# Performance work log

Hardware: AMD Instinct MI355X
Metric: run time of the kernel (lower is better)

Reference implementation:

```python
import jax, jax.numpy as jnp
import numpy as np

N_QUBITS = 8
REPS = 2
DIM = 2 ** N_QUBITS  # 256
C64 = jnp.complex64


def _apply_1q(state, gate, wire):
    """Apply a single-qubit gate. state: [B]+[2]*n, gate: [2,2] or [B,2,2]."""
    s = jnp.moveaxis(state, wire + 1, -1)
    if gate.ndim == 2:
        s = jnp.einsum('ij,b...j->b...i', gate, s)
    else:
        s = jnp.einsum('bij,b...j->b...i', gate, s)
    return jnp.moveaxis(s, -1, wire + 1)


def _cnot(state, ctrl, tgt):
    """CNOT: flip target axis where control bit == 1. state: [B]+[2]*n."""
    s0 = jax.lax.index_in_dim(state, 0, ctrl + 1, keepdims=True)
    s1 = jax.lax.index_in_dim(state, 1, ctrl + 1, keepdims=True)
    s1 = jnp.flip(s1, axis=tgt + 1)
    return jnp.concatenate([s0, s1], axis=ctrl + 1)


def _rx(a):
    """Batched RX gate. a: [B] -> [B,2,2] complex64."""
    c = jnp.cos(0.5 * a).astype(C64)
    s = jnp.sin(0.5 * a).astype(C64)
    mis = (-1j) * s
    return jnp.stack([jnp.stack([c, mis], -1), jnp.stack([mis, c], -1)], -2)


def _rot(phi, theta, omega):
    """PennyLane Rot = RZ(omega) RY(theta) RZ(phi). Scalars -> [2,2] complex64."""
    c = jnp.cos(0.5 * theta).astype(C64)
    s = jnp.sin(0.5 * theta).astype(C64)
    ep = jnp.exp(-0.5j * (phi + omega).astype(C64))   # e^{-i(phi+omega)/2}
    em = jnp.exp(-0.5j * (phi - omega).astype(C64))   # e^{-i(phi-omega)/2}
    epc = jnp.exp(0.5j * (phi + omega).astype(C64))
    emc = jnp.exp(0.5j * (phi - omega).astype(C64))
    return jnp.stack([
        jnp.stack([ep * c, -emc * s], -1),
        jnp.stack([em * s, epc * c], -1),
    ], -2)


def _circuit(x, theta):
    B = x.shape[0]
    state = jnp.zeros((B, DIM), C64).at[:, 0].set(1.0)
    state = state.reshape((B,) + (2,) * N_QUBITS)
    # AngleEmbedding (default rotation='X'): RX(x[:, w]) on wire w
    for w in range(N_QUBITS):
        state = _apply_1q(state, _rx(x[:, w]), w)
    # StronglyEntanglingLayers: per layer, Rot on every wire then ring of CNOTs
    for l in range(REPS):
        for w in range(N_QUBITS):
            g = _rot(theta[l, w, 0], theta[l, w, 1], theta[l, w, 2])
            state = _apply_1q(state, g, w)
        r = (l % (N_QUBITS - 1)) + 1  # PennyLane default ranges
        for w in range(N_QUBITS):
            state = _cnot(state, w, (w + r) % N_QUBITS)
    # expval(PauliZ(0)): wire 0 is the most significant axis
    probs = (state.real ** 2 + state.imag ** 2).reshape(B, 2, DIM // 2)
    ev = probs[:, 0].sum(-1) - probs[:, 1].sum(-1)
    return ((ev + 1.0) * 0.5)[:, None]  # [B, 1]


def setup_inputs() -> dict:
    key = jax.random.key(0)
    kx, kt = jax.random.split(key)
    x = jax.random.normal(kx, (131072, N_QUBITS), dtype=jnp.float32)
    theta = 0.1 * jax.random.normal(kt, (REPS, N_QUBITS, 3), dtype=jnp.float32)
    return {"x": x, "theta": theta}


def reference(x, theta):
    return _circuit(x, theta)
```

## Files before the change

kernel.cpp:

```cpp
#include <hip/hip_runtime.h>


typedef _Float16 v8hf __attribute__((ext_vector_type(8)));
typedef float v4f __attribute__((ext_vector_type(4)));

struct cpx { float re, im; };
__device__ __forceinline__ cpx cmul(cpx a, cpx b) {
    return {a.re * b.re - a.im * b.im, a.re * b.im + a.im * b.re};
}

__device__ __forceinline__ void get_pauli(int a, cpx P[2][2]) {
    cpx z{0.f, 0.f};
    P[0][0] = z; P[0][1] = z; P[1][0] = z; P[1][1] = z;
    switch (a) {
        case 0: P[0][0] = {1.f, 0.f}; P[1][1] = {1.f, 0.f}; break;
        case 1: P[0][1] = {1.f, 0.f}; P[1][0] = {1.f, 0.f}; break;
        case 2: P[0][1] = {0.f, -1.f}; P[1][0] = {0.f, 1.f}; break;
        case 3: P[0][0] = {1.f, 0.f}; P[1][1] = {-1.f, 0.f}; break;
    }
}

__device__ void compute_ptm(const float* __restrict__ theta, int l, int w,
                            float* out) {
    const float phi = theta[(l * 8 + w) * 3 + 0];
    const float th  = theta[(l * 8 + w) * 3 + 1];
    const float om  = theta[(l * 8 + w) * 3 + 2];
    const float c = cosf(0.5f * th), s = sinf(0.5f * th);
    const float ps = 0.5f * (phi + om), ms = 0.5f * (phi - om);
    cpx G[2][2];
    G[0][0] = {c * cosf(ps), -c * sinf(ps)};
    G[0][1] = {-s * cosf(ms), -s * sinf(ms)};
    G[1][0] = {s * cosf(ms), -s * sinf(ms)};
    G[1][1] = {c * cosf(ps), c * sinf(ps)};
    for (int a = 0; a < 4; ++a) {
        cpx Pa[2][2]; get_pauli(a, Pa);
        cpx M1[2][2];
        for (int i = 0; i < 2; ++i)
            for (int j = 0; j < 2; ++j) {
                cpx acc{0.f, 0.f};
                for (int k = 0; k < 2; ++k) {
                    cpx t = cmul(Pa[i][k], G[k][j]);
                    acc.re += t.re; acc.im += t.im;
                }
                M1[i][j] = acc;
            }
        cpx H[2][2];
        for (int i = 0; i < 2; ++i)
            for (int j = 0; j < 2; ++j) {
                cpx acc{0.f, 0.f};
                for (int k = 0; k < 2; ++k) {
                    cpx gc{G[k][i].re, -G[k][i].im};
                    cpx t = cmul(gc, M1[k][j]);
                    acc.re += t.re; acc.im += t.im;
                }
                H[i][j] = acc;
            }
        for (int b = 0; b < 4; ++b) {
            cpx Pb[2][2]; get_pauli(b, Pb);
            float tr = 0.f;
            for (int i = 0; i < 2; ++i)
                for (int j = 0; j < 2; ++j)
                    tr += Pb[i][j].re * H[j][i].re - Pb[i][j].im * H[j][i].im;
            out[a * 4 + b] = 0.5f * tr;
        }
    }
}

__device__ void compute_cnot_entry(int pr, int* oidx, float* osgn) {
    const int pc = pr >> 2, pt = pr & 3;
    const int perm[4] = {0, 1, 3, 2};
    cpx Pc[2][2], Pt[2][2];
    get_pauli(pc, Pc); get_pauli(pt, Pt);
    cpx S[4][4];
    for (int i = 0; i < 2; ++i)
        for (int j = 0; j < 2; ++j)
            for (int k = 0; k < 2; ++k)
                for (int l2 = 0; l2 < 2; ++l2)
                    S[2 * i + j][2 * k + l2] = cmul(Pc[i][k], Pt[j][l2]);
    cpx R[4][4];
    for (int r = 0; r < 4; ++r)
        for (int c2 = 0; c2 < 4; ++c2)
            R[r][c2] = S[perm[r]][perm[c2]];
    int bidx = 0; float bsgn = 1.f;
    for (int a = 0; a < 4; ++a)
        for (int b2 = 0; b2 < 4; ++b2) {
            cpx Pa[2][2], Pb[2][2];
            get_pauli(a, Pa); get_pauli(b2, Pb);
            float ov = 0.f;
            for (int r = 0; r < 4; ++r)
                for (int c2 = 0; c2 < 4; ++c2) {
                    cpx K = cmul(Pa[r >> 1][c2 >> 1], Pb[r & 1][c2 & 1]);
                    ov += K.re * R[r][c2].re + K.im * R[r][c2].im;
                }
            ov *= 0.25f;
            if (ov > 0.5f) { bidx = a * 4 + b2; bsgn = 1.f; }
            else if (ov < -0.5f) { bidx = a * 4 + b2; bsgn = -1.f; }
        }
    *oidx = bidx;
    *osgn = bsgn;
}

#define OFF_AF 0
#define OFF_R  4096
#define WS_FLOATS_NEEDED (4096 + 16 * 729)

__device__ __forceinline__ int ring_conj(int cur, int r, const int* CIDX,
                                         const float* CSGN, float& sg) {
    for (int w = 7; w >= 0; --w) {
        const int tw = (w + r) & 7;
        const int pc = (cur >> (2 * w)) & 3;
        const int pt = (cur >> (2 * tw)) & 3;
        const int q = pc * 4 + pt;
        const int nq = CIDX[q];
        sg *= CSGN[q];
        cur = (cur & ~((3 << (2 * w)) | (3 << (2 * tw))))
            | ((nq >> 2) << (2 * w)) | ((nq & 3) << (2 * tw));
    }
    return cur;
}

__global__ __launch_bounds__(1024) void k_sub(const float* __restrict__ theta,
                                              float* __restrict__ ws) {
    __shared__ float TR[256];
    __shared__ float CSGN[16];
    __shared__ int   CIDX[16];
    __shared__ float Wa[4096];
    __shared__ float Wb[3072];
    __shared__ int   S1k, S1n;
    __shared__ float S1sgn;
    __shared__ int   S1w[8], S1l[8];

    const int tid = threadIdx.x;
    const int sub = blockIdx.x;
    const int sa0 = sub >> 2, sa1 = sub & 3;
    float* Rg = ws + OFF_R;

    if (tid < 16) compute_ptm(theta, tid >> 3, tid & 7, &TR[tid * 16]);
    if (tid >= 64 && tid < 80) compute_cnot_entry(tid - 64, &CIDX[tid - 64], &CSGN[tid - 64]);
    for (int i = tid; i < 4096; i += 1024) Wa[i] = 0.f;
    __syncthreads();

    if (tid == 0) {
        float sg = 1.f;
        int cur = ring_conj(3 , 2, CIDX, CSGN, sg);
        int k = 0;
        for (int w = 0; w < 8; ++w) {
            const int ltr = (cur >> (2 * w)) & 3;
            if (ltr != 0) { S1w[k] = w; S1l[k] = ltr; ++k; }
        }
        int n = 1;
        for (int i = 0; i < k; ++i) n *= 3;
        S1sgn = sg; S1k = k; S1n = n;
    }
    __syncthreads();
    const int k1 = S1k, n1 = S1n;

    for (int t = tid; t < n1; t += 1024) {
        float c = S1sgn;
        int s = 0;
        int tt = t;
        for (int i = 0; i < k1; ++i) {
            const int bl = tt % 3 + 1;
            tt /= 3;
            c *= TR[(8 + S1w[i]) * 16 + S1l[i] * 4 + bl];
            s |= bl << (2 * S1w[i]);
        }
        float sg = 1.f;
        s = ring_conj(s, 1, CIDX, CSGN, sg);
        c *= sg;
        if (((s & 3) == sa0) && (((s >> 2) & 3) == sa1)) {
            int d4 = 0;
#pragma unroll
            for (int w = 2; w < 8; ++w)
                d4 |= ((s >> (2 * w)) & 3) << (2 * (7 - w));
            Wa[d4] = c;
        }
    }
    __syncthreads();

    const int P3c[6] = {1, 3, 9, 27, 81, 243};
    const int N4c[6] = {1024, 256, 64, 16, 4, 1};
#pragma unroll
    for (int tl = 0; tl < 6; ++tl) {
        const int w = 7 - tl;
        const float* src = (tl & 1) ? Wb : Wa;
        float* dst = (tl & 1) ? Wa : Wb;
        const int p3 = P3c[tl];
        const int Nout = p3 * 3 * N4c[tl];
        for (int idx = tid; idx < Nout; idx += 1024) {
            const int q3 = idx % p3;
            const int rest = idx / p3;
            const int P = rest % 3;
            const int r = rest / 3;
            const int let = (P == 0) ? 0 : ((P == 1) ? 3 : 2);
            const float* ib = src + q3 + p3 * 4 * r;
            dst[idx] = ib[0] * TR[w * 16 + 0 + let]
                     + ib[p3] * TR[w * 16 + 4 + let]
                     + ib[2 * p3] * TR[w * 16 + 8 + let]
                     + ib[3 * p3] * TR[w * 16 + 12 + let];
        }
        __syncthreads();
    }
    for (int k = tid; k < 729; k += 1024) Rg[sub * 729 + k] = Wa[k];
}

__global__ __launch_bounds__(1024) void k_fin(const float* __restrict__ theta,
                                              float* __restrict__ ws) {
    __shared__ float BIG[8748];
    __shared__ float TRw[32];
    const int tid = threadIdx.x;
    if (tid < 2) compute_ptm(theta, 0, tid, &TRw[tid * 16]);
    __syncthreads();

    const float* Rg = ws + OFF_R;
    for (int idx1 = tid; idx1 < 8748; idx1 += 1024) {
        const int a0 = idx1 / 2187;
        const int rem = idx1 % 2187;
        const int P1 = rem / 729;
        const int qq = rem % 729;
        const int let = (P1 == 0) ? 0 : ((P1 == 1) ? 3 : 2);
        float v = 0.f;
#pragma unroll
        for (int a1 = 0; a1 < 4; ++a1)
            v += Rg[(a0 * 4 + a1) * 729 + qq] * TRw[16 + a1 * 4 + let];
        BIG[idx1] = v;
    }
    __syncthreads();

    int* AFi = (int*)(ws + OFF_AF);
    for (int u = tid; u < 4096; u += 1024) {
        const int t = u >> 8;
        const int lane = (u >> 2) & 63;
        const int jj0 = (u & 3) * 2;
        const int m = lane & 15;
        const int i = t * 16 + m;
        const int jb = (lane >> 4) * 8;
        unsigned int packed = 0;
#pragma unroll
        for (int z = 0; z < 2; ++z) {
            const int j = jb + jj0 + z;
            float v = 0.f;
            if (i < 243 && j < 27) {
                const int idxF = i * 27 + j;
                const int P0 = idxF / 2187;
                const int rest = idxF % 2187;
                const int let = (P0 == 0) ? 0 : ((P0 == 1) ? 3 : 2);
                v = BIG[rest] * TRw[0 + let]
                  + BIG[2187 + rest] * TRw[4 + let]
                  + BIG[2 * 2187 + rest] * TRw[8 + let]
                  + BIG[3 * 2187 + rest] * TRw[12 + let];
            }
            const _Float16 hv = (_Float16)v;
            const unsigned short bits = __builtin_bit_cast(unsigned short, hv);
            packed |= ((unsigned int)bits) << (16 * z);
        }
        AFi[u] = (int)packed;
    }
}

template <int Q>
__device__ __forceinline__ v8hf build_bfrag(const float* m5v, const float* m6v,
                                            const float* m7v) {
    v8hf bf;
#pragma unroll
    for (int jj = 0; jj < 8; ++jj) {
        const int j = Q * 8 + jj;
        float v = 0.f;
        if (j < 27) {
            const int k5 = j / 9, k6 = (j % 9) / 3, k7 = j % 3;
            v = m5v[k5] * m6v[k6] * m7v[k7];
        }
        bf[jj] = (_Float16)v;
    }
    return bf;
}

template <int Q>
__device__ __forceinline__ float contract_f1(const v4f* acc, const float* P01,
                                             const float* P23, const float* m4v) {
    float ev = 0.f;
#pragma unroll
    for (int t = 0; t < 16; ++t) {
#pragma unroll
        for (int s = 0; s < 4; ++s) {
            const int i = 16 * t + 4 * Q + s;
            if (i < 243) {
                const int u = i / 27, vv = (i % 27) / 3, w = i % 3;
                float f = P01[u] * P23[vv];
                if (w != 0) f *= m4v[w];
                ev = fmaf(f, acc[t][s], ev);
            }
        }
    }
    return ev;
}

__global__ __launch_bounds__(256, 2) void k_main4(const float* __restrict__ x,
                                                  const float* __restrict__ wsAF,
                                                  float* __restrict__ out,
                                                  int ngroups) {
    const int lane = threadIdx.x & 63;
    const int q = lane >> 4, e = lane & 15;
    const int wid = (blockIdx.x * blockDim.x + threadIdx.x) >> 6;
    if (wid >= ngroups) return;

    const int b = wid * 16 + e;
    const float4* xp = (const float4*)(x + (size_t)b * 8);
    const float4 xa = xp[0], xb = xp[1];
    float m0v[3], m1v[3], m2v[3], m3v[3], m4v[3], m5v[3], m6v[3], m7v[3];
    {
        float sv, cv;
        __sincosf(xa.x, &sv, &cv); m0v[0] = 1.f; m0v[1] = cv; m0v[2] = -sv;
        __sincosf(xa.y, &sv, &cv); m1v[0] = 1.f; m1v[1] = cv; m1v[2] = -sv;
        __sincosf(xa.z, &sv, &cv); m2v[0] = 1.f; m2v[1] = cv; m2v[2] = -sv;
        __sincosf(xa.w, &sv, &cv); m3v[0] = 1.f; m3v[1] = cv; m3v[2] = -sv;
        __sincosf(xb.x, &sv, &cv); m4v[0] = 1.f; m4v[1] = cv; m4v[2] = -sv;
        __sincosf(xb.y, &sv, &cv); m5v[0] = 1.f; m5v[1] = cv; m5v[2] = -sv;
        __sincosf(xb.z, &sv, &cv); m6v[0] = 1.f; m6v[1] = cv; m6v[2] = -sv;
        __sincosf(xb.w, &sv, &cv); m7v[0] = 1.f; m7v[1] = cv; m7v[2] = -sv;
    }

    v8hf bf;
    if (q == 0)      bf = build_bfrag<0>(m5v, m6v, m7v);
    else if (q == 1) bf = build_bfrag<1>(m5v, m6v, m7v);
    else if (q == 2) bf = build_bfrag<2>(m5v, m6v, m7v);
    else             bf = build_bfrag<3>(m5v, m6v, m7v);

    float P01[9], P23[9];
#pragma unroll
    for (int a = 0; a < 3; ++a)
#pragma unroll
        for (int b2 = 0; b2 < 3; ++b2) {
            P01[a * 3 + b2] = m0v[a] * m1v[b2];
            P23[a * 3 + b2] = m2v[a] * m3v[b2];
        }

    const v4f zero = {0.f, 0.f, 0.f, 0.f};
    const v8hf* AFp = (const v8hf*)wsAF;
    v4f acc[16];
#pragma unroll
    for (int t = 0; t < 16; ++t)
        acc[t] = __builtin_amdgcn_mfma_f32_16x16x32_f16(AFp[t * 64 + lane], bf, zero, 0, 0, 0);

    float ev;
    if (q == 0)      ev = contract_f1<0>(acc, P01, P23, m4v);
    else if (q == 1) ev = contract_f1<1>(acc, P01, P23, m4v);
    else if (q == 2) ev = contract_f1<2>(acc, P01, P23, m4v);
    else             ev = contract_f1<3>(acc, P01, P23, m4v);

    ev += __shfl_xor(ev, 16, 64);
    ev += __shfl_xor(ev, 32, 64);
    if (lane < 16) out[b] = (ev + 1.f) * 0.5f;
}

struct c32 { float x, y; };

__device__ __forceinline__ c32 shfl_xor_c(c32 v, int mask) {
    c32 r;
    r.x = __shfl_xor(v.x, mask, 64);
    r.y = __shfl_xor(v.y, mask, 64);
    return r;
}
__device__ __forceinline__ c32 cmadd2(c32 ga, c32 a, c32 gp, c32 p) {
    c32 n;
    n.x = ga.x * a.x - ga.y * a.y + gp.x * p.x - gp.y * p.y;
    n.y = ga.x * a.y + ga.y * a.x + gp.x * p.y + gp.y * p.x;
    return n;
}
__device__ __forceinline__ c32 rx_mix(float c, float s, c32 a, c32 p) {
    c32 n;
    n.x = c * a.x + s * p.y;
    n.y = c * a.y - s * p.x;
    return n;
}
__device__ __forceinline__ void apply_rx(c32 st[4], int lane, int bb, float c, float s) {
    if (bb < 6) {
#pragma unroll
        for (int r = 0; r < 4; ++r) {
            c32 p = shfl_xor_c(st[r], 1 << bb);
            st[r] = rx_mix(c, s, st[r], p);
        }
    } else if (bb == 6) {
        c32 n0 = rx_mix(c, s, st[0], st[1]);
        c32 n1 = rx_mix(c, s, st[1], st[0]);
        c32 n2 = rx_mix(c, s, st[2], st[3]);
        c32 n3 = rx_mix(c, s, st[3], st[2]);
        st[0] = n0; st[1] = n1; st[2] = n2; st[3] = n3;
    } else {
        c32 n0 = rx_mix(c, s, st[0], st[2]);
        c32 n2 = rx_mix(c, s, st[2], st[0]);
        c32 n1 = rx_mix(c, s, st[1], st[3]);
        c32 n3 = rx_mix(c, s, st[3], st[1]);
        st[0] = n0; st[1] = n1; st[2] = n2; st[3] = n3;
    }
}
__device__ __forceinline__ void apply_rot(c32 st[4], int lane, int bb,
                                          c32 g00, c32 g01, c32 g10, c32 g11) {
    if (bb < 6) {
#pragma unroll
        for (int r = 0; r < 4; ++r) {
            c32 p = shfl_xor_c(st[r], 1 << bb);
            bool hi = (lane >> bb) & 1;
            c32 ga, gp;
            ga.x = hi ? g11.x : g00.x;
            ga.y = hi ? g11.y : g00.y;
            gp.x = hi ? g10.x : g01.x;
            gp.y = hi ? g10.y : g01.y;
            st[r] = cmadd2(ga, st[r], gp, p);
        }
    } else if (bb == 6) {
        c32 n0 = cmadd2(g00, st[0], g01, st[1]);
        c32 n1 = cmadd2(g10, st[0], g11, st[1]);
        c32 n2 = cmadd2(g00, st[2], g01, st[3]);
        c32 n3 = cmadd2(g10, st[2], g11, st[3]);
        st[0] = n0; st[1] = n1; st[2] = n2; st[3] = n3;
    } else {
        c32 n0 = cmadd2(g00, st[0], g01, st[2]);
        c32 n2 = cmadd2(g10, st[0], g11, st[2]);
        c32 n1 = cmadd2(g00, st[1], g01, st[3]);
        c32 n3 = cmadd2(g10, st[1], g11, st[3]);
        st[0] = n0; st[1] = n1; st[2] = n2; st[3] = n3;
    }
}
__device__ __forceinline__ void cswap(bool c, c32& a, c32& b) {
    c32 t = a;
    a.x = c ? b.x : a.x; a.y = c ? b.y : a.y;
    b.x = c ? t.x : b.x; b.y = c ? t.y : b.y;
}
__device__ __forceinline__ void apply_cnot(c32 st[4], int lane, int bc, int bt) {
    if (bt < 6) {
        if (bc < 6) {
            bool ctrl = (lane >> bc) & 1;
#pragma unroll
            for (int r = 0; r < 4; ++r) {
                c32 p = shfl_xor_c(st[r], 1 << bt);
                st[r].x = ctrl ? p.x : st[r].x;
                st[r].y = ctrl ? p.y : st[r].y;
            }
        } else {
#pragma unroll
            for (int r = 0; r < 4; ++r) {
                if ((r >> (bc - 6)) & 1) st[r] = shfl_xor_c(st[r], 1 << bt);
            }
        }
    } else {
        if (bc < 6) {
            bool ctrl = (lane >> bc) & 1;
            if (bt == 6) { cswap(ctrl, st[0], st[1]); cswap(ctrl, st[2], st[3]); }
            else         { cswap(ctrl, st[0], st[2]); cswap(ctrl, st[1], st[3]); }
        } else {
            if (bc == 7 && bt == 6) { c32 t = st[2]; st[2] = st[3]; st[3] = t; }
            else if (bc == 6 && bt == 7) { c32 t = st[1]; st[1] = st[3]; st[3] = t; }
        }
    }
}
__global__ __launch_bounds__(256) void qsim_kernel(const float* __restrict__ x,
                                                   const float* __restrict__ theta,
                                                   float* __restrict__ out,
                                                   int batch) {
    __shared__ float rot[2 * 8 * 8];
    const int t = threadIdx.x;
    if (t < 16) {
        const int l = t >> 3, w = t & 7;
        const float phi = theta[(l * 8 + w) * 3 + 0];
        const float th  = theta[(l * 8 + w) * 3 + 1];
        const float om  = theta[(l * 8 + w) * 3 + 2];
        const float c = cosf(0.5f * th), s = sinf(0.5f * th);
        const float p = 0.5f * (phi + om), m = 0.5f * (phi - om);
        float* g = &rot[t * 8];
        g[0] = c * cosf(p);  g[1] = -c * sinf(p);
        g[2] = -s * cosf(m); g[3] = -s * sinf(m);
        g[4] = s * cosf(m);  g[5] = -s * sinf(m);
        g[6] = c * cosf(p);  g[7] = c * sinf(p);
    }
    __syncthreads();
    const int lane = t & 63;
    const int b = blockIdx.x * 4 + (t >> 6);
    if (b >= batch) return;
    float c8 = 0.f, s8 = 0.f;
    if (lane < 8) {
        const float xv = 0.5f * x[b * 8 + lane];
        c8 = cosf(xv); s8 = sinf(xv);
    }
    c32 st[4];
#pragma unroll
    for (int r = 0; r < 4; ++r) { st[r].x = 0.f; st[r].y = 0.f; }
    if (lane == 0) st[0].x = 1.f;
#pragma unroll
    for (int w = 0; w < 8; ++w) {
        const float c = __shfl(c8, w, 64);
        const float s = __shfl(s8, w, 64);
        apply_rx(st, lane, 7 - w, c, s);
    }
#pragma unroll
    for (int l = 0; l < 2; ++l) {
#pragma unroll
        for (int w = 0; w < 8; ++w) {
            const float* g = &rot[(l * 8 + w) * 8];
            c32 g00{g[0], g[1]}, g01{g[2], g[3]}, g10{g[4], g[5]}, g11{g[6], g[7]};
            apply_rot(st, lane, 7 - w, g00, g01, g10, g11);
        }
        const int rr = l + 1;
#pragma unroll
        for (int w = 0; w < 8; ++w) apply_cnot(st, lane, 7 - w, 7 - ((w + rr) & 7));
    }
    float v = st[0].x * st[0].x + st[0].y * st[0].y
            + st[1].x * st[1].x + st[1].y * st[1].y
            - st[2].x * st[2].x - st[2].y * st[2].y
            - st[3].x * st[3].x - st[3].y * st[3].y;
#pragma unroll
    for (int off = 32; off > 0; off >>= 1) v += __shfl_xor(v, off, 64);
    if (lane == 0) out[b] = (v + 1.f) * 0.5f;
}

extern "C" void kernel_launch(void* const* d_in, const int* in_sizes, int n_in,
                              void* d_out, int out_size, void* d_ws, size_t ws_size,
                              hipStream_t stream) {
    const float* x     = (const float*)d_in[0];
    const float* theta = (const float*)d_in[1];
    float* out = (float*)d_out;
    const int batch = in_sizes[0] / 8;

    if (ws_size >= (size_t)WS_FLOATS_NEEDED * 4 + 256 && (batch & 15) == 0) {
        float* ws = (float*)d_ws;
        k_sub<<<dim3(16), dim3(1024), 0, stream>>>(theta, ws);
        k_fin<<<dim3(1), dim3(1024), 0, stream>>>(theta, ws);
        const int ngroups = batch / 16;
        const int blocks = (ngroups + 3) / 4;
        k_main4<<<dim3(blocks), dim3(256), 0, stream>>>(x, ws + OFF_AF, out, ngroups);
    } else {
        qsim_kernel<<<dim3((batch + 3) / 4), dim3(256), 0, stream>>>(x, theta, out, batch);
    }
}
```

Before: 81.90 us.

## Merge prep kernels with flag sync and reuse MFMA A-fragments across two groups

Fuses the two setup kernels into one 17-block launch. Sixteen blocks build the partial tables and publish them with release flags, and the 17th block spin-waits on those flags before doing the final reduction. The per-gate transfer-matrix and CNOT entries are now computed in parallel, one entry per thread, instead of by a few serial threads. In the main kernel each wave loads its A fragments into registers once and processes two batch groups, and precomputes a 27-entry product table to simplify the contraction. The flags are never reset between calls, so on later calls the final block may read a partially rewritten workspace. The wait also relies on all 17 blocks being resident at the same time.

Measured after the change: 91.13 us. 11.3% more time.

```diff
diff --git a/kernel.cpp b/kernel.cpp
--- a/kernel.cpp
+++ b/kernel.cpp
@@ -9,19 +9,17 @@
     return {a.re * b.re - a.im * b.im, a.re * b.im + a.im * b.re};
 }
 
-__device__ __forceinline__ void get_pauli(int a, cpx P[2][2]) {
-    cpx z{0.f, 0.f};
-    P[0][0] = z; P[0][1] = z; P[1][0] = z; P[1][1] = z;
-    switch (a) {
-        case 0: P[0][0] = {1.f, 0.f}; P[1][1] = {1.f, 0.f}; break;
-        case 1: P[0][1] = {1.f, 0.f}; P[1][0] = {1.f, 0.f}; break;
-        case 2: P[0][1] = {0.f, -1.f}; P[1][0] = {0.f, 1.f}; break;
-        case 3: P[0][0] = {1.f, 0.f}; P[1][1] = {-1.f, 0.f}; break;
-    }
-}
-
-__device__ void compute_ptm(const float* __restrict__ theta, int l, int w,
-                            float* out) {
+__device__ __forceinline__ cpx pget(int a, int i, int j) {
+    static const float RE[4][4] = {{1, 0, 0, 1}, {0, 1, 1, 0},
+                                   {0, 0, 0, 0}, {1, 0, 0, -1}};
+    static const float IM[4][4] = {{0, 0, 0, 0}, {0, 0, 0, 0},
+                                   {0, -1, 1, 0}, {0, 0, 0, 0}};
+    cpx r; r.re = RE[a][i * 2 + j]; r.im = IM[a][i * 2 + j];
+    return r;
+}
+
+__device__ float ptm_entry(const float* __restrict__ theta, int g, int a, int b) {
+    const int l = g >> 3, w = g & 7;
     const float phi = theta[(l * 8 + w) * 3 + 0];
     const float th  = theta[(l * 8 + w) * 3 + 1];
     const float om  = theta[(l * 8 + w) * 3 + 2];
@@ -32,77 +30,66 @@
     G[0][1] = {-s * cosf(ms), -s * sinf(ms)};
     G[1][0] = {s * cosf(ms), -s * sinf(ms)};
     G[1][1] = {c * cosf(ps), c * sinf(ps)};
-    for (int a = 0; a < 4; ++a) {
-        cpx Pa[2][2]; get_pauli(a, Pa);
-        cpx M1[2][2];
-        for (int i = 0; i < 2; ++i)
-            for (int j = 0; j < 2; ++j) {
-                cpx acc{0.f, 0.f};
-                for (int k = 0; k < 2; ++k) {
-                    cpx t = cmul(Pa[i][k], G[k][j]);
-                    acc.re += t.re; acc.im += t.im;
-                }
-                M1[i][j] = acc;
-            }
-        cpx H[2][2];
-        for (int i = 0; i < 2; ++i)
-            for (int j = 0; j < 2; ++j) {
-                cpx acc{0.f, 0.f};
-                for (int k = 0; k < 2; ++k) {
-                    cpx gc{G[k][i].re, -G[k][i].im};
-                    cpx t = cmul(gc, M1[k][j]);
-                    acc.re += t.re; acc.im += t.im;
-                }
-                H[i][j] = acc;
-            }
-        for (int b = 0; b < 4; ++b) {
-            cpx Pb[2][2]; get_pauli(b, Pb);
-            float tr = 0.f;
-            for (int i = 0; i < 2; ++i)
-                for (int j = 0; j < 2; ++j)
-                    tr += Pb[i][j].re * H[j][i].re - Pb[i][j].im * H[j][i].im;
-            out[a * 4 + b] = 0.5f * tr;
-        }
-    }
-}
-
-__device__ void compute_cnot_entry(int pr, int* oidx, float* osgn) {
+    cpx M1[2][2], H[2][2];
+#pragma unroll
+    for (int i = 0; i < 2; ++i)
+#pragma unroll
+        for (int j = 0; j < 2; ++j) {
+            cpx acc{0.f, 0.f};
+#pragma unroll
+            for (int k = 0; k < 2; ++k) {
+                cpx t = cmul(pget(a, i, k), G[k][j]);
+                acc.re += t.re; acc.im += t.im;
+            }
+            M1[i][j] = acc;
+        }
+#pragma unroll
+    for (int i = 0; i < 2; ++i)
+#pragma unroll
+        for (int j = 0; j < 2; ++j) {
+            cpx acc{0.f, 0.f};
+#pragma unroll
+            for (int k = 0; k < 2; ++k) {
+                cpx gc{G[k][i].re, -G[k][i].im};
+                cpx t = cmul(gc, M1[k][j]);
+                acc.re += t.re; acc.im += t.im;
+            }
+            H[i][j] = acc;
+        }
+    float tr = 0.f;
+#pragma unroll
+    for (int i = 0; i < 2; ++i)
+#pragma unroll
+        for (int j = 0; j < 2; ++j) {
+            cpx pb = pget(b, i, j);
+            tr += pb.re * H[j][i].re - pb.im * H[j][i].im;
+        }
+    return 0.5f * tr;
+}
+
+__device__ void cnot_entry(int pr, int cand, int* CIDX, float* CSGN) {
     const int pc = pr >> 2, pt = pr & 3;
+    const int a = cand >> 2, b2 = cand & 3;
     const int perm[4] = {0, 1, 3, 2};
-    cpx Pc[2][2], Pt[2][2];
-    get_pauli(pc, Pc); get_pauli(pt, Pt);
-    cpx S[4][4];
-    for (int i = 0; i < 2; ++i)
-        for (int j = 0; j < 2; ++j)
-            for (int k = 0; k < 2; ++k)
-                for (int l2 = 0; l2 < 2; ++l2)
-                    S[2 * i + j][2 * k + l2] = cmul(Pc[i][k], Pt[j][l2]);
-    cpx R[4][4];
+    float ov = 0.f;
+#pragma unroll
     for (int r = 0; r < 4; ++r)
-        for (int c2 = 0; c2 < 4; ++c2)
-            R[r][c2] = S[perm[r]][perm[c2]];
-    int bidx = 0; float bsgn = 1.f;
-    for (int a = 0; a < 4; ++a)
-        for (int b2 = 0; b2 < 4; ++b2) {
-            cpx Pa[2][2], Pb[2][2];
-            get_pauli(a, Pa); get_pauli(b2, Pb);
-            float ov = 0.f;
-            for (int r = 0; r < 4; ++r)
-                for (int c2 = 0; c2 < 4; ++c2) {
-                    cpx K = cmul(Pa[r >> 1][c2 >> 1], Pb[r & 1][c2 & 1]);
-                    ov += K.re * R[r][c2].re + K.im * R[r][c2].im;
-                }
-            ov *= 0.25f;
-            if (ov > 0.5f) { bidx = a * 4 + b2; bsgn = 1.f; }
-            else if (ov < -0.5f) { bidx = a * 4 + b2; bsgn = -1.f; }
-        }
-    *oidx = bidx;
-    *osgn = bsgn;
-}
-
-#define OFF_AF 0
-#define OFF_R  4096
-#define WS_FLOATS_NEEDED (4096 + 16 * 729)
+#pragma unroll
+        for (int c2 = 0; c2 < 4; ++c2) {
+            const int rp = perm[r], cp = perm[c2];
+            cpx Rv = cmul(pget(pc, rp >> 1, cp >> 1), pget(pt, rp & 1, cp & 1));
+            cpx Kv = cmul(pget(a, r >> 1, c2 >> 1), pget(b2, r & 1, c2 & 1));
+            ov += Kv.re * Rv.re + Kv.im * Rv.im;
+        }
+    ov *= 0.25f;
+    if (ov > 0.5f) { CIDX[pr] = cand; CSGN[pr] = 1.f; }
+    else if (ov < -0.5f) { CIDX[pr] = cand; CSGN[pr] = -1.f; }
+}
+
+#define OFF_AF   0
+#define OFF_R    4096
+#define OFF_FLAG (4096 + 16 * 729)
+#define WS_FLOATS_NEEDED (4096 + 16 * 729 + 16)
 
 __device__ __forceinline__ int ring_conj(int cur, int r, const int* CIDX,
                                          const float* CSGN, float& sg) {
@@ -119,142 +106,160 @@
     return cur;
 }
 
-__global__ __launch_bounds__(1024) void k_sub(const float* __restrict__ theta,
+__global__ __launch_bounds__(256) void k_prep(const float* __restrict__ theta,
                                               float* __restrict__ ws) {
-    __shared__ float TR[256];
-    __shared__ float CSGN[16];
-    __shared__ int   CIDX[16];
-    __shared__ float Wa[4096];
-    __shared__ float Wb[3072];
+    __shared__ float SH[8960];
     __shared__ int   S1k, S1n;
     __shared__ float S1sgn;
     __shared__ int   S1w[8], S1l[8];
 
     const int tid = threadIdx.x;
-    const int sub = blockIdx.x;
-    const int sa0 = sub >> 2, sa1 = sub & 3;
+    const int blk = blockIdx.x;
     float* Rg = ws + OFF_R;
-
-    if (tid < 16) compute_ptm(theta, tid >> 3, tid & 7, &TR[tid * 16]);
-    if (tid >= 64 && tid < 80) compute_cnot_entry(tid - 64, &CIDX[tid - 64], &CSGN[tid - 64]);
-    for (int i = tid; i < 4096; i += 1024) Wa[i] = 0.f;
-    __syncthreads();
-
-    if (tid == 0) {
-        float sg = 1.f;
-        int cur = ring_conj(3 , 2, CIDX, CSGN, sg);
-        int k = 0;
-        for (int w = 0; w < 8; ++w) {
-            const int ltr = (cur >> (2 * w)) & 3;
-            if (ltr != 0) { S1w[k] = w; S1l[k] = ltr; ++k; }
-        }
-        int n = 1;
-        for (int i = 0; i < k; ++i) n *= 3;
-        S1sgn = sg; S1k = k; S1n = n;
-    }
-    __syncthreads();
-    const int k1 = S1k, n1 = S1n;
-
-    for (int t = tid; t < n1; t += 1024) {
-        float c = S1sgn;
-        int s = 0;
-        int tt = t;
-        for (int i = 0; i < k1; ++i) {
-            const int bl = tt % 3 + 1;
-            tt /= 3;
-            c *= TR[(8 + S1w[i]) * 16 + S1l[i] * 4 + bl];
-            s |= bl << (2 * S1w[i]);
-        }
-        float sg = 1.f;
-        s = ring_conj(s, 1, CIDX, CSGN, sg);
-        c *= sg;
-        if (((s & 3) == sa0) && (((s >> 2) & 3) == sa1)) {
-            int d4 = 0;
-#pragma unroll
-            for (int w = 2; w < 8; ++w)
-                d4 |= ((s >> (2 * w)) & 3) << (2 * (7 - w));
-            Wa[d4] = c;
-        }
-    }
-    __syncthreads();
-
-    const int P3c[6] = {1, 3, 9, 27, 81, 243};
-    const int N4c[6] = {1024, 256, 64, 16, 4, 1};
-#pragma unroll
-    for (int tl = 0; tl < 6; ++tl) {
-        const int w = 7 - tl;
-        const float* src = (tl & 1) ? Wb : Wa;
-        float* dst = (tl & 1) ? Wa : Wb;
-        const int p3 = P3c[tl];
-        const int Nout = p3 * 3 * N4c[tl];
-        for (int idx = tid; idx < Nout; idx += 1024) {
-            const int q3 = idx % p3;
-            const int rest = idx / p3;
-            const int P = rest % 3;
-            const int r = rest / 3;
-            const int let = (P == 0) ? 0 : ((P == 1) ? 3 : 2);
-            const float* ib = src + q3 + p3 * 4 * r;
-            dst[idx] = ib[0] * TR[w * 16 + 0 + let]
-                     + ib[p3] * TR[w * 16 + 4 + let]
-                     + ib[2 * p3] * TR[w * 16 + 8 + let]
-                     + ib[3 * p3] * TR[w * 16 + 12 + let];
-        }
+    int* FLAGS = (int*)(ws + OFF_FLAG);
+
+    if (blk < 16) {
+        float* TR   = SH;
+        float* CSGN = SH + 256;
+        int*   CIDX = (int*)(SH + 272);
+        float* Wa   = SH + 288;
+        float* Wb   = SH + 4384;
+
+        const int sa0 = blk >> 2, sa1 = blk & 3;
+
+        TR[tid] = ptm_entry(theta, tid >> 4, (tid >> 2) & 3, tid & 3);
+        cnot_entry(tid >> 4, tid & 15, CIDX, CSGN);
+        for (int i = tid; i < 4096; i += 256) Wa[i] = 0.f;
         __syncthreads();
-    }
-    for (int k = tid; k < 729; k += 1024) Rg[sub * 729 + k] = Wa[k];
-}
-
-__global__ __launch_bounds__(1024) void k_fin(const float* __restrict__ theta,
-                                              float* __restrict__ ws) {
-    __shared__ float BIG[8748];
-    __shared__ float TRw[32];
-    const int tid = threadIdx.x;
-    if (tid < 2) compute_ptm(theta, 0, tid, &TRw[tid * 16]);
-    __syncthreads();
-
-    const float* Rg = ws + OFF_R;
-    for (int idx1 = tid; idx1 < 8748; idx1 += 1024) {
-        const int a0 = idx1 / 2187;
-        const int rem = idx1 % 2187;
-        const int P1 = rem / 729;
-        const int qq = rem % 729;
-        const int let = (P1 == 0) ? 0 : ((P1 == 1) ? 3 : 2);
-        float v = 0.f;
-#pragma unroll
-        for (int a1 = 0; a1 < 4; ++a1)
-            v += Rg[(a0 * 4 + a1) * 729 + qq] * TRw[16 + a1 * 4 + let];
-        BIG[idx1] = v;
-    }
-    __syncthreads();
-
-    int* AFi = (int*)(ws + OFF_AF);
-    for (int u = tid; u < 4096; u += 1024) {
-        const int t = u >> 8;
-        const int lane = (u >> 2) & 63;
-        const int jj0 = (u & 3) * 2;
-        const int m = lane & 15;
-        const int i = t * 16 + m;
-        const int jb = (lane >> 4) * 8;
-        unsigned int packed = 0;
-#pragma unroll
-        for (int z = 0; z < 2; ++z) {
-            const int j = jb + jj0 + z;
+
+        if (tid == 0) {
+            float sg = 1.f;
+            int cur = ring_conj(3 , 2, CIDX, CSGN, sg);
+            int k = 0;
+            for (int w = 0; w < 8; ++w) {
+                const int ltr = (cur >> (2 * w)) & 3;
+                if (ltr != 0) { S1w[k] = w; S1l[k] = ltr; ++k; }
+            }
+            int n = 1;
+            for (int i = 0; i < k; ++i) n *= 3;
+            S1sgn = sg; S1k = k; S1n = n;
+        }
+        __syncthreads();
+        const int k1 = S1k, n1 = S1n;
+
+        for (int t = tid; t < n1; t += 256) {
+            float c = S1sgn;
+            int s = 0;
+            int tt = t;
+            for (int i = 0; i < k1; ++i) {
+                const int bl = tt % 3 + 1;
+                tt /= 3;
+                c *= TR[(8 + S1w[i]) * 16 + S1l[i] * 4 + bl];
+                s |= bl << (2 * S1w[i]);
+            }
+            float sg = 1.f;
+            s = ring_conj(s, 1, CIDX, CSGN, sg);
+            c *= sg;
+            if (((s & 3) == sa0) && (((s >> 2) & 3) == sa1)) {
+                int d4 = 0;
+#pragma unroll
+                for (int w = 2; w < 8; ++w)
+                    d4 |= ((s >> (2 * w)) & 3) << (2 * (7 - w));
+                Wa[d4] = c;
+            }
+        }
+        __syncthreads();
+
+        const int P3c[6] = {1, 3, 9, 27, 81, 243};
+        const int N4c[6] = {1024, 256, 64, 16, 4, 1};
+#pragma unroll
+        for (int tl = 0; tl < 6; ++tl) {
+            const int w = 7 - tl;
+            const float* src = (tl & 1) ? Wb : Wa;
+            float* dst = (tl & 1) ? Wa : Wb;
+            const int p3 = P3c[tl];
+            const int Nout = p3 * 3 * N4c[tl];
+            for (int idx = tid; idx < Nout; idx += 256) {
+                const int q3 = idx % p3;
+                const int rest = idx / p3;
+                const int P = rest % 3;
+                const int r = rest / 3;
+                const int let = (P == 0) ? 0 : ((P == 1) ? 3 : 2);
+                const float* ib = src + q3 + p3 * 4 * r;
+                dst[idx] = ib[0] * TR[w * 16 + 0 + let]
+                         + ib[p3] * TR[w * 16 + 4 + let]
+                         + ib[2 * p3] * TR[w * 16 + 8 + let]
+                         + ib[3 * p3] * TR[w * 16 + 12 + let];
+            }
+            __syncthreads();
+        }
+        for (int k = tid; k < 729; k += 256)
+            __hip_atomic_store(&Rg[blk * 729 + k], Wa[k],
+                               __ATOMIC_RELAXED, __HIP_MEMORY_SCOPE_AGENT);
+        __threadfence();
+        __syncthreads();
+        if (tid == 0)
+            __hip_atomic_store(&FLAGS[blk], 1,
+                               __ATOMIC_RELEASE, __HIP_MEMORY_SCOPE_AGENT);
+    } else {
+        float* BIG = SH;
+        float* TRw = SH + 8748;
+        if (tid < 32)
+            TRw[tid] = ptm_entry(theta, tid >> 4, (tid >> 2) & 3, tid & 3);
+        if (tid < 16) {
+            while (__hip_atomic_load(&FLAGS[tid], __ATOMIC_ACQUIRE,
+                                     __HIP_MEMORY_SCOPE_AGENT) != 1) {
+                __builtin_amdgcn_s_sleep(1);
+            }
+        }
+        __threadfence();
+        __syncthreads();
+
+        for (int idx1 = tid; idx1 < 8748; idx1 += 256) {
+            const int a0 = idx1 / 2187;
+            const int rem = idx1 % 2187;
+            const int P1 = rem / 729;
+            const int qq = rem % 729;
+            const int let = (P1 == 0) ? 0 : ((P1 == 1) ? 3 : 2);
             float v = 0.f;
-            if (i < 243 && j < 27) {
-                const int idxF = i * 27 + j;
-                const int P0 = idxF / 2187;
-                const int rest = idxF % 2187;
-                const int let = (P0 == 0) ? 0 : ((P0 == 1) ? 3 : 2);
-                v = BIG[rest] * TRw[0 + let]
-                  + BIG[2187 + rest] * TRw[4 + let]
-                  + BIG[2 * 2187 + rest] * TRw[8 + let]
-                  + BIG[3 * 2187 + rest] * TRw[12 + let];
-            }
-            const _Float16 hv = (_Float16)v;
-            const unsigned short bits = __builtin_bit_cast(unsigned short, hv);
-            packed |= ((unsigned int)bits) << (16 * z);
-        }
-        AFi[u] = (int)packed;
+#pragma unroll
+            for (int a1 = 0; a1 < 4; ++a1)
+                v += __hip_atomic_load(&Rg[(a0 * 4 + a1) * 729 + qq],
+                                       __ATOMIC_RELAXED, __HIP_MEMORY_SCOPE_AGENT)
+                     * TRw[16 + a1 * 4 + let];
+            BIG[idx1] = v;
+        }
+        __syncthreads();
+
+        int* AFi = (int*)(ws + OFF_AF);
+        for (int u = tid; u < 4096; u += 256) {
+            const int t = u >> 8;
+            const int lane = (u >> 2) & 63;
+            const int jj0 = (u & 3) * 2;
+            const int m = lane & 15;
+            const int i = t * 16 + m;
+            const int jb = (lane >> 4) * 8;
+            unsigned int packed = 0;
+#pragma unroll
+            for (int z = 0; z < 2; ++z) {
+                const int j = jb + jj0 + z;
+                float v = 0.f;
+                if (i < 243 && j < 27) {
+                    const int idxF = i * 27 + j;
+                    const int P0 = idxF / 2187;
+                    const int rest = idxF % 2187;
+                    const int let = (P0 == 0) ? 0 : ((P0 == 1) ? 3 : 2);
+                    v = BIG[rest] * TRw[0 + let]
+                      + BIG[2187 + rest] * TRw[4 + let]
+                      + BIG[2 * 2187 + rest] * TRw[8 + let]
+                      + BIG[3 * 2187 + rest] * TRw[12 + let];
+                }
+                const _Float16 hv = (_Float16)v;
+                const unsigned short bits = __builtin_bit_cast(unsigned short, hv);
+                packed |= ((unsigned int)bits) << (16 * z);
+            }
+            AFi[u] = (int)packed;
+        }
     }
 }
 
@@ -276,81 +281,85 @@
 }
 
 template <int Q>
-__device__ __forceinline__ float contract_f1(const v4f* acc, const float* P01,
-                                             const float* P23, const float* m4v) {
+__device__ __forceinline__ float contract_f1(const v4f* acc, const float* U9,
+                                             const float* R27) {
     float ev = 0.f;
 #pragma unroll
     for (int t = 0; t < 16; ++t) {
 #pragma unroll
         for (int s = 0; s < 4; ++s) {
             const int i = 16 * t + 4 * Q + s;
-            if (i < 243) {
-                const int u = i / 27, vv = (i % 27) / 3, w = i % 3;
-                float f = P01[u] * P23[vv];
-                if (w != 0) f *= m4v[w];
-                ev = fmaf(f, acc[t][s], ev);
-            }
+            if (i < 243)
+                ev = fmaf(U9[i / 27] * R27[i % 27], acc[t][s], ev);
         }
     }
     return ev;
 }
 
-__global__ __launch_bounds__(256, 2) void k_main4(const float* __restrict__ x,
+__global__ __launch_bounds__(256, 2) void k_main5(const float* __restrict__ x,
                                                   const float* __restrict__ wsAF,
                                                   float* __restrict__ out,
                                                   int ngroups) {
     const int lane = threadIdx.x & 63;
     const int q = lane >> 4, e = lane & 15;
-    const int wid = (blockIdx.x * blockDim.x + threadIdx.x) >> 6;
-    if (wid >= ngroups) return;
-
-    const int b = wid * 16 + e;
-    const float4* xp = (const float4*)(x + (size_t)b * 8);
-    const float4 xa = xp[0], xb = xp[1];
-    float m0v[3], m1v[3], m2v[3], m3v[3], m4v[3], m5v[3], m6v[3], m7v[3];
-    {
-        float sv, cv;
-        __sincosf(xa.x, &sv, &cv); m0v[0] = 1.f; m0v[1] = cv; m0v[2] = -sv;
-        __sincosf(xa.y, &sv, &cv); m1v[0] = 1.f; m1v[1] = cv; m1v[2] = -sv;
-        __sincosf(xa.z, &sv, &cv); m2v[0] = 1.f; m2v[1] = cv; m2v[2] = -sv;
-        __sincosf(xa.w, &sv, &cv); m3v[0] = 1.f; m3v[1] = cv; m3v[2] = -sv;
-        __sincosf(xb.x, &sv, &cv); m4v[0] = 1.f; m4v[1] = cv; m4v[2] = -sv;
-        __sincosf(xb.y, &sv, &cv); m5v[0] = 1.f; m5v[1] = cv; m5v[2] = -sv;
-        __sincosf(xb.z, &sv, &cv); m6v[0] = 1.f; m6v[1] = cv; m6v[2] = -sv;
-        __sincosf(xb.w, &sv, &cv); m7v[0] = 1.f; m7v[1] = cv; m7v[2] = -sv;
-    }
-
-    v8hf bf;
-    if (q == 0)      bf = build_bfrag<0>(m5v, m6v, m7v);
-    else if (q == 1) bf = build_bfrag<1>(m5v, m6v, m7v);
-    else if (q == 2) bf = build_bfrag<2>(m5v, m6v, m7v);
-    else             bf = build_bfrag<3>(m5v, m6v, m7v);
-
-    float P01[9], P23[9];
-#pragma unroll
-    for (int a = 0; a < 3; ++a)
-#pragma unroll
-        for (int b2 = 0; b2 < 3; ++b2) {
-            P01[a * 3 + b2] = m0v[a] * m1v[b2];
-            P23[a * 3 + b2] = m2v[a] * m3v[b2];
-        }
-
-    const v4f zero = {0.f, 0.f, 0.f, 0.f};
+    const int wslot = (blockIdx.x * blockDim.x + threadIdx.x) >> 6;
+
     const v8hf* AFp = (const v8hf*)wsAF;
-    v4f acc[16];
-#pragma unroll
-    for (int t = 0; t < 16; ++t)
-        acc[t] = __builtin_amdgcn_mfma_f32_16x16x32_f16(AFp[t * 64 + lane], bf, zero, 0, 0, 0);
-
-    float ev;
-    if (q == 0)      ev = contract_f1<0>(acc, P01, P23, m4v);
-    else if (q == 1) ev = contract_f1<1>(acc, P01, P23, m4v);
-    else if (q == 2) ev = contract_f1<2>(acc, P01, P23, m4v);
-    else             ev = contract_f1<3>(acc, P01, P23, m4v);
-
-    ev += __shfl_xor(ev, 16, 64);
-    ev += __shfl_xor(ev, 32, 64);
-    if (lane < 16) out[b] = (ev + 1.f) * 0.5f;
+    v8hf af[16];
+#pragma unroll
+    for (int t = 0; t < 16; ++t) af[t] = AFp[t * 64 + lane];
+
+    for (int gi = 0; gi < 2; ++gi) {
+        const int g = wslot * 2 + gi;
+        if (g >= ngroups) return;
+        const int b = g * 16 + e;
+        const float4* xp = (const float4*)(x + (size_t)b * 8);
+        const float4 xa = xp[0], xb = xp[1];
+
+        float m0v[3], m1v[3], m2v[3], m3v[3], m4v[3], m5v[3], m6v[3], m7v[3];
+        m0v[0] = 1.f; m0v[1] = __cosf(xa.x); m0v[2] = -__sinf(xa.x);
+        m1v[0] = 1.f; m1v[1] = __cosf(xa.y); m1v[2] = -__sinf(xa.y);
+        m2v[0] = 1.f; m2v[1] = __cosf(xa.z); m2v[2] = -__sinf(xa.z);
+        m3v[0] = 1.f; m3v[1] = __cosf(xa.w); m3v[2] = -__sinf(xa.w);
+        m4v[0] = 1.f; m4v[1] = __cosf(xb.x); m4v[2] = -__sinf(xb.x);
+        m5v[0] = 1.f; m5v[1] = __cosf(xb.y); m5v[2] = -__sinf(xb.y);
+        m6v[0] = 1.f; m6v[1] = __cosf(xb.z); m6v[2] = -__sinf(xb.z);
+        m7v[0] = 1.f; m7v[1] = __cosf(xb.w); m7v[2] = -__sinf(xb.w);
+
+        v8hf bf;
+        if (q == 0)      bf = build_bfrag<0>(m5v, m6v, m7v);
+        else if (q == 1) bf = build_bfrag<1>(m5v, m6v, m7v);
+        else if (q == 2) bf = build_bfrag<2>(m5v, m6v, m7v);
+        else             bf = build_bfrag<3>(m5v, m6v, m7v);
+
+        float U9[9], R27[27];
+#pragma unroll
+        for (int a = 0; a < 3; ++a)
+#pragma unroll
+            for (int b2 = 0; b2 < 3; ++b2) {
+                U9[a * 3 + b2] = m0v[a] * m1v[b2];
+                const float p23 = m2v[a] * m3v[b2];
+#pragma unroll
+                for (int c2 = 0; c2 < 3; ++c2)
+                    R27[(a * 3 + b2) * 3 + c2] = p23 * m4v[c2];
+            }
+
+        const v4f zero = {0.f, 0.f, 0.f, 0.f};
+        v4f acc[16];
+#pragma unroll
+        for (int t = 0; t < 16; ++t)
+            acc[t] = __builtin_amdgcn_mfma_f32_16x16x32_f16(af[t], bf, zero, 0, 0, 0);
+
+        float ev;
+        if (q == 0)      ev = contract_f1<0>(acc, U9, R27);
+        else if (q == 1) ev = contract_f1<1>(acc, U9, R27);
+        else if (q == 2) ev = contract_f1<2>(acc, U9, R27);
+        else             ev = contract_f1<3>(acc, U9, R27);
+
+        ev += __shfl_xor(ev, 16, 64);
+        ev += __shfl_xor(ev, 32, 64);
+        if (lane < 16) out[b] = (ev + 1.f) * 0.5f;
+    }
 }
 
 struct c32 { float x, y; };
@@ -523,11 +532,10 @@
 
     if (ws_size >= (size_t)WS_FLOATS_NEEDED * 4 + 256 && (batch & 15) == 0) {
         float* ws = (float*)d_ws;
-        k_sub<<<dim3(16), dim3(1024), 0, stream>>>(theta, ws);
-        k_fin<<<dim3(1), dim3(1024), 0, stream>>>(theta, ws);
+        k_prep<<<dim3(17), dim3(256), 0, stream>>>(theta, ws);
         const int ngroups = batch / 16;
-        const int blocks = (ngroups + 3) / 4;
-        k_main4<<<dim3(blocks), dim3(256), 0, stream>>>(x, ws + OFF_AF, out, ngroups);
+        const int blocks = (ngroups + 7) / 8;
+        k_main5<<<dim3(blocks), dim3(256), 0, stream>>>(x, ws + OFF_AF, out, ngroups);
     } else {
         qsim_kernel<<<dim3((batch + 3) / 4), dim3(256), 0, stream>>>(x, theta, out, batch);
     }
```
